# Performance work log

Hardware: AMD Instinct MI355X
Metric: run time of the kernel (lower is better)

The kernel has to match this reference:

```python
import math
import jax, jax.numpy as jnp
import numpy as np

HIDDEN = 128
NUM_REL = 48
NUM_BASES = 8
NUM_ENT = 50000
NUM_SPECIAL = 64
NUM_EDGES = 600000


def setup_inputs() -> dict:
    key = jax.random.key(0)
    ks = jax.random.split(key, 8)
    edge_index = jax.random.randint(ks[0], (2, NUM_EDGES), 0, NUM_ENT, dtype=jnp.int64)
    edge_type = jax.random.randint(ks[1], (NUM_EDGES,), 0, NUM_REL, dtype=jnp.int64)
    # node embeddings: uniform(-stdv, stdv), stdv = sqrt(6/(N+d)) as in the torch init
    stdv = math.sqrt(6.0 / (NUM_ENT + HIDDEN))
    node_embeds = jax.random.uniform(ks[2], (NUM_ENT, HIDDEN), jnp.float32, -stdv, stdv)
    # RGCN basis-decomposition params (PyG RGCNConv): weight [B, d, d], comp [R, B]
    basis = jax.random.normal(ks[3], (NUM_BASES, HIDDEN, HIDDEN), jnp.float32) * (1.0 / math.sqrt(HIDDEN))
    comp = jax.random.normal(ks[4], (NUM_REL, NUM_BASES), jnp.float32) * (1.0 / math.sqrt(NUM_BASES))
    root = jax.random.normal(ks[5], (HIDDEN, HIDDEN), jnp.float32) * (1.0 / math.sqrt(HIDDEN))
    bias = jnp.zeros((HIDDEN,), jnp.float32)
    special_emb = jax.random.normal(ks[6], (NUM_SPECIAL, HIDDEN), jnp.float32) * 0.02
    special_emb = special_emb.at[0].set(0.0)  # padding_idx=0
    return {"edge_index": edge_index, "edge_type": edge_type,
            "node_embeds": node_embeds, "basis": basis, "comp": comp,
            "root": root, "bias": bias, "special_emb": special_emb}


def rgcn_conv(x, edge_index, edge_type, basis, comp, root, bias):
    # PyG RGCNConv with basis decomposition, aggr='mean', root weight + bias.
    # W_r = sum_b comp[r, b] * basis[b]; out[n] = x[n] @ root + bias
    #        + sum_r mean_{e: type(e)=r, dst(e)=n} (x[src(e)] @ W_r)
    N = x.shape[0]
    R, B = comp.shape
    src, dst = edge_index[0], edge_index[1]
    # per-(relation, dst) in-degree for the per-relation mean aggregation
    seg = edge_type * N + dst  # [E]
    cnt = jax.ops.segment_sum(jnp.ones(src.shape[0], x.dtype), seg, num_segments=R * N)
    norm = 1.0 / jnp.maximum(cnt[seg], 1.0)  # [E]
    w = comp[edge_type] * norm[:, None]  # [E, B] per-edge basis coefficients / count
    x_src = x[src]  # [E, d] gather (dominant memory traffic)
    out = x @ root + bias  # [N, d]
    # linearity: mean over edges of (x_src @ W) == (weighted-sum of x_src) @ basis_b per basis
    for b in range(B):
        agg = jax.ops.segment_sum(x_src * w[:, b:b + 1], dst, num_segments=N)  # [N, d]
        out = out + agg @ basis[b]
    return out


def reference(edge_index, edge_type, node_embeds, basis, comp, root, bias, special_emb):
    node_out = rgcn_conv(node_embeds, edge_index, edge_type, basis, comp, root, bias)
    return jnp.concatenate([node_out, special_emb], axis=0)  # [N + S, d]
```

## Files before the change

### kernel.cpp

```cpp
#include <hip/hip_runtime.h>

#define NDIM 128
#define NBASES 8
#define KDIM 1152
#define GTILE 16
#define APITCH 1160

typedef __attribute__((ext_vector_type(8))) __bf16 bfrag;
typedef __attribute__((ext_vector_type(4))) float f32x4;

__device__ __forceinline__ float bf2f(unsigned short b) {
    return __uint_as_float(((unsigned)b) << 16);
}
__device__ __forceinline__ unsigned short f2bf(float f) {
    unsigned u = __float_as_uint(f);
    unsigned r = u + 0x7FFFu + ((u >> 16) & 1u);
    return (unsigned short)(r >> 16);
}
__device__ __forceinline__ unsigned pack2bf(float lo, float hi) {
    return (unsigned)f2bf(lo) | ((unsigned)f2bf(hi) << 16);
}
__device__ __forceinline__ float loadF(const void* p, int idx, int isf32) {
    return isf32 ? ((const float*)p)[idx] : bf2f(((const unsigned short*)p)[idx]);
}

__global__ void detect_k(const unsigned short* __restrict__ xs,
                         const int* __restrict__ ei, int* __restrict__ meta) {
    if (threadIdx.x != 0 || blockIdx.x != 0) return;
    const uint4* xv = (const uint4*)xs;
    unsigned f32m = 0;
    uint4 bx[16];
    #pragma unroll
    for (int i = 0; i < 16; ++i) bx[i] = xv[i];
    #pragma unroll
    for (int i = 0; i < 16; ++i) {
        unsigned a = bx[i].x, b = bx[i].y, c = bx[i].z, d = bx[i].w;
        f32m |= (((a & 0xFFFFu) >> 7) & 0xFFu) > 124u;
        f32m |= (((b & 0xFFFFu) >> 7) & 0xFFu) > 124u;
        f32m |= (((c & 0xFFFFu) >> 7) & 0xFFu) > 124u;
        f32m |= (((d & 0xFFFFu) >> 7) & 0xFFu) > 124u;
    }
    const uint4* ev = (const uint4*)ei;
    unsigned nzm = 0;
    for (int r = 0; r < 4; ++r) {
        uint4 be[16];
        #pragma unroll
        for (int i = 0; i < 16; ++i) be[i] = ev[r * 16 + i];
        #pragma unroll
        for (int i = 0; i < 16; ++i) nzm |= be[i].y | be[i].w;
    }
    meta[0] = f32m ? 1 : 0;
    meta[1] = nzm ? 0 : 1;
}

__global__ void misc_k(const void* __restrict__ basis, const void* __restrict__ root,
                       const void* __restrict__ se, const int* __restrict__ meta,
                       unsigned short* __restrict__ BT, void* __restrict__ out,
                       int scount, int sbase,
                       const int* __restrict__ ei, int E, int N, int* __restrict__ hist) {
    int t = blockIdx.x * 256 + threadIdx.x;
    int isf32 = meta[0];
    if (t < NDIM * KDIM) {
        int j = t / KDIM, k = t % KDIM;
        float v = (k < NBASES * NDIM) ? loadF(basis, k * NDIM + j, isf32)
                                      : loadF(root, (k - NBASES * NDIM) * NDIM + j, isf32);
        BT[t] = f2bf(v);
    } else {
        int u = t - NDIM * KDIM;
        if (u < scount) {
            float v = loadF(se, u, isf32);
            if (isf32) ((float*)out)[sbase + u] = v;
            else       ((unsigned short*)out)[sbase + u] = f2bf(v);
        } else {
            int e = u - scount;
            if (e < E) {
                int dst = meta[1] ? ei[2 * (E + e)] : ei[E + e];
                dst = min(max(dst, 0), N - 1);
                atomicAdd(&hist[dst], 1);
            }
        }
    }
}

__global__ void scanA_k(const int* __restrict__ hist, int N,
                        int* __restrict__ offsets, int* __restrict__ bsum) {
    __shared__ int s[1024];
    int tid = threadIdx.x;
    int idx = blockIdx.x * 1024 + tid;
    int v = (idx < N) ? hist[idx] : 0;
    s[tid] = v;
    __syncthreads();
    for (int off = 1; off < 1024; off <<= 1) {
        int t = 0;
        if (tid >= off) t = s[tid - off];
        __syncthreads();
        if (tid >= off) s[tid] += t;
        __syncthreads();
    }
    if (idx < N) offsets[idx] = s[tid] - v;
    if (tid == 1023) bsum[blockIdx.x] = s[1023];
}
__global__ void scanB_k(const int* __restrict__ bsum, int NB, int N,
                        int* __restrict__ bpre, int* __restrict__ offsets) {
    __shared__ int s[64];
    int tid = threadIdx.x;
    int v = (tid < NB) ? bsum[tid] : 0;
    s[tid] = v;
    __syncthreads();
    for (int off = 1; off < 64; off <<= 1) {
        int t = 0;
        if (tid >= off) t = s[tid - off];
        __syncthreads();
        if (tid >= off) s[tid] += t;
        __syncthreads();
    }
    if (tid < NB) bpre[tid] = s[tid] - v;
    if (tid == NB - 1) offsets[N] = s[tid];
}

__global__ void scatter_k(const int* __restrict__ ei, const int* __restrict__ et,
                          int E, int N, const int* __restrict__ meta,
                          const int* __restrict__ offsets, const int* __restrict__ bpre,
                          int* __restrict__ cursor, int* __restrict__ sorted) {
    int e = blockIdx.x * 256 + threadIdx.x;
    if (e >= E) return;
    int i64 = meta[1];
    int src = i64 ? ei[2 * e] : ei[e];
    int dst = i64 ? ei[2 * (E + e)] : ei[E + e];
    int rel = i64 ? et[2 * e] : et[e];
    src = min(max(src, 0), N - 1);
    dst = min(max(dst, 0), N - 1);
    rel = rel & 63;
    int pos = offsets[dst] + bpre[dst >> 10] + atomicAdd(&cursor[dst], 1);
    sorted[pos] = src | (rel << 16);
}

__global__ __launch_bounds__(1024, 8) void rgcn_main_k(
    const void* __restrict__ x, const void* __restrict__ comp,
    const void* __restrict__ bias, const unsigned short* __restrict__ BT,
    const int* __restrict__ meta, const int* __restrict__ offsets,
    const int* __restrict__ bpre,
    const int* __restrict__ sorted, void* __restrict__ out, int N)
{
    __shared__ alignas(16) unsigned short A_lds[GTILE * APITCH];
    __shared__ alignas(16) float comp_lds[48 * NBASES];
    __shared__ int cnt_lds[GTILE * 48];
    const int tid  = threadIdx.x;
    const int lane = tid & 63;
    const int wave = tid >> 6;
    const int isf32 = meta[0];

    for (int t = tid; t < 48 * NBASES; t += 1024)
        comp_lds[t] = loadF(comp, t, isf32);
    __syncthreads();

    const int nodeBase = blockIdx.x * GTILE;
    const int dl = lane & 31;
    const int eg = lane >> 5;

    {
        const int n = nodeBase + wave;
        float acc[4][4];
        #pragma unroll
        for (int b = 0; b < 4; ++b)
            #pragma unroll
            for (int i = 0; i < 4; ++i) acc[b][i] = 0.f;

        int* cnt_row = &cnt_lds[wave * 48];

        if (n < N) {
            const int start = offsets[n] + bpre[n >> 10];
            const int idx1  = n + 1;
            const int end   = offsets[idx1] + ((idx1 < N) ? bpre[idx1 >> 10] : 0);

            if (lane < 48) cnt_row[lane] = 0;
            for (int c = start + lane; c < end; c += 64)
                atomicAdd(&cnt_row[(sorted[c] >> 16) & 63], 1);
            if (lane < 48) {
                float nv = __builtin_amdgcn_rcpf(fmaxf((float)cnt_row[lane], 1.0f));
                cnt_row[lane] = __float_as_int(nv);
            }

            if (!isf32) {
                const unsigned short* xh = (const unsigned short*)x;
                if (start < end) {
                    int i0 = start + eg;
                    unsigned q0 = (i0 < end) ? (unsigned)sorted[i0] : 0u;
                    int i1 = start + 2 + eg;
                    unsigned q1 = (i1 < end) ? (unsigned)sorted[i1] : 0u;
                    uint2 xa0 = *(const uint2*)(xh + (size_t)(q0 & 0xFFFFu) * NDIM + dl * 4);
                    uint2 xa1 = *(const uint2*)(xh + (size_t)(q1 & 0xFFFFu) * NDIM + dl * 4);
                    int i2 = start + 4 + eg;
                    unsigned q2 = (i2 < end) ? (unsigned)sorted[i2] : 0u;
                    for (int c = start; c < end; c += 2) {
                        uint2 xa2 = *(const uint2*)(xh + (size_t)(q2 & 0xFFFFu) * NDIM + dl * 4);
                        int i3 = c + 6 + eg;
                        unsigned q3 = (i3 < end) ? (unsigned)sorted[i3] : 0u;

                        bool act_o = (c + eg) < end;
                        bool act_p = (c + (1 ^ eg)) < end;
                        unsigned qp = (unsigned)__shfl_xor((int)q0, 32);
                        int rel_o = (int)((q0 >> 16) & 63u);
                        int rel_p = (int)((qp >> 16) & 63u);
                        float nrm_o = act_o ? __int_as_float(cnt_row[rel_o]) : 0.f;
                        float nrm_p = act_p ? __int_as_float(cnt_row[rel_p]) : 0.f;
                        f32x4 cw_o = *(const f32x4*)&comp_lds[rel_o * NBASES + 4 * eg];
                        f32x4 cw_p = *(const f32x4*)&comp_lds[rel_p * NBASES + 4 * eg];
                        unsigned px = (unsigned)__shfl_xor((int)xa0.x, 32);
                        unsigned py = (unsigned)__shfl_xor((int)xa0.y, 32);
                        float xo[4], xq[4];
                        xo[0] = __uint_as_float(xa0.x << 16)          * nrm_o;
                        xo[1] = __uint_as_float(xa0.x & 0xFFFF0000u)  * nrm_o;
                        xo[2] = __uint_as_float(xa0.y << 16)          * nrm_o;
                        xo[3] = __uint_as_float(xa0.y & 0xFFFF0000u)  * nrm_o;
                        xq[0] = __uint_as_float(px << 16)             * nrm_p;
                        xq[1] = __uint_as_float(px & 0xFFFF0000u)     * nrm_p;
                        xq[2] = __uint_as_float(py << 16)             * nrm_p;
                        xq[3] = __uint_as_float(py & 0xFFFF0000u)     * nrm_p;
                        #pragma unroll
                        for (int b = 0; b < 4; ++b)
                            #pragma unroll
                            for (int i = 0; i < 4; ++i)
                                acc[b][i] += cw_o[b] * xo[i] + cw_p[b] * xq[i];
                        q0 = q1; q1 = q2; q2 = q3;
                        xa0 = xa1; xa1 = xa2;
                    }
                }
            } else {
                const float* xfp = (const float*)x;
                for (int c = start; c < end; c += 2) {
                    bool act_o = (c + eg) < end;
                    bool act_p = (c + (1 ^ eg)) < end;
                    int io = c + eg;
                    unsigned q0 = (io < end) ? (unsigned)sorted[io] : 0u;
                    unsigned qp = (unsigned)__shfl_xor((int)q0, 32);
                    int rel_o = (int)((q0 >> 16) & 63u);
                    int rel_p = (int)((qp >> 16) & 63u);
                    float nrm_o = act_o ? __int_as_float(cnt_row[rel_o]) : 0.f;
                    float nrm_p = act_p ? __int_as_float(cnt_row[rel_p]) : 0.f;
                    f32x4 cw_o = *(const f32x4*)&comp_lds[rel_o * NBASES + 4 * eg];
                    f32x4 cw_p = *(const f32x4*)&comp_lds[rel_p * NBASES + 4 * eg];
                    f32x4 xv = *(const f32x4*)(xfp + (size_t)(q0 & 0xFFFFu) * NDIM + dl * 4);
                    float xo[4], xq[4];
                    #pragma unroll
                    for (int i = 0; i < 4; ++i) {
                        xo[i] = xv[i] * nrm_o;
                        xq[i] = __shfl_xor(xv[i], 32) * nrm_p;
                    }
                    #pragma unroll
                    for (int b = 0; b < 4; ++b)
                        #pragma unroll
                        for (int i = 0; i < 4; ++i)
                            acc[b][i] += cw_o[b] * xo[i] + cw_p[b] * xq[i];
                }
            }
        }

        unsigned short* row = &A_lds[wave * APITCH];
        #pragma unroll
        for (int b = 0; b < 4; ++b) {
            uint2 p;
            p.x = pack2bf(acc[b][0], acc[b][1]);
            p.y = pack2bf(acc[b][2], acc[b][3]);
            *(uint2*)(row + (4 * eg + b) * NDIM + dl * 4) = p;
        }
        if (eg == 0) {
            uint2 xr = {0, 0};
            if (n < N) {
                if (!isf32) {
                    xr = *(const uint2*)((const unsigned short*)x + (size_t)n * NDIM + dl * 4);
                } else {
                    const float* xf = (const float*)x + (size_t)n * NDIM + dl * 4;
                    xr.x = pack2bf(xf[0], xf[1]);
                    xr.y = pack2bf(xf[2], xf[3]);
                }
            }
            *(uint2*)(row + NBASES * NDIM + dl * 4) = xr;
        }
    }
    __syncthreads();

    if (wave < 4) {
        const int m = lane & 15;
        const int q = lane >> 4;
        f32x4 C0 = {0,0,0,0}, C1 = {0,0,0,0};
        const unsigned short* arow = &A_lds[m * APITCH];
        const int jb = wave * 32;
        for (int ks = 0; ks < KDIM / 32; ++ks) {
            int k = ks * 32 + q * 8;
            bfrag a  = *(const bfrag*)(arow + k);
            bfrag b0 = *(const bfrag*)(BT + (size_t)(jb +  0 + m) * KDIM + k);
            bfrag b1 = *(const bfrag*)(BT + (size_t)(jb + 16 + m) * KDIM + k);
            C0 = __builtin_amdgcn_mfma_f32_16x16x32_bf16(a, b0, C0, 0, 0, 0);
            C1 = __builtin_amdgcn_mfma_f32_16x16x32_bf16(a, b1, C1, 0, 0, 0);
        }
        #pragma unroll
        for (int t = 0; t < 2; ++t) {
            f32x4 Ct = t ? C1 : C0;
            int j = jb + t * 16 + m;
            float bj = loadF(bias, j, isf32);
            #pragma unroll
            for (int r = 0; r < 4; ++r) {
                int n = nodeBase + q * 4 + r;
                if (n < N) {
                    float v = Ct[r] + bj;
                    if (isf32) ((float*)out)[(size_t)n * NDIM + j] = v;
                    else       ((unsigned short*)out)[(size_t)n * NDIM + j] = f2bf(v);
                }
            }
        }
    }
}

extern "C" void kernel_launch(void* const* d_in, const int* in_sizes, int n_in,
                              void* d_out, int out_size, void* d_ws, size_t ws_size,
                              hipStream_t stream) {
    const int* ei = (const int*)d_in[0];
    const int* et = (const int*)d_in[1];

    const int E = in_sizes[1];
    const int N = in_sizes[2] / NDIM;
    const int S = in_sizes[7] / NDIM;
    const int NB = (N + 1023) / 1024;

    char* ws = (char*)d_ws;
    size_t off = 0;
    int* meta    = (int*)(ws + off); off += 16;
    int* hist    = (int*)(ws + off); off += (size_t)N * 4;
    int* cursor  = (int*)(ws + off); off += (size_t)N * 4;
    int* offsets = (int*)(ws + off); off = (off + (size_t)(N + 1) * 4 + 15) & ~(size_t)15;
    int* bsum    = (int*)(ws + off); off += 64 * 4;
    int* bpre    = (int*)(ws + off); off += 64 * 4;
    unsigned short* BT = (unsigned short*)(ws + off); off += (size_t)NDIM * KDIM * 2;
    int* sorted  = (int*)(ws + off); off += (size_t)E * 4;

    hipMemsetAsync(hist, 0, (size_t)2 * N * 4, stream);

    detect_k<<<1, 64, 0, stream>>>((const unsigned short*)d_in[2], ei, meta);
    {
        int T = NDIM * KDIM + S * NDIM + E;
        misc_k<<<(T + 255) / 256, 256, 0, stream>>>(
            d_in[3], d_in[5], d_in[7], meta, BT, d_out, S * NDIM, N * NDIM,
            ei, E, N, hist);
    }
    scanA_k<<<NB, 1024, 0, stream>>>(hist, N, offsets, bsum);
    scanB_k<<<1, 64, 0, stream>>>(bsum, NB, N, bpre, offsets);
    scatter_k<<<(E + 255) / 256, 256, 0, stream>>>(ei, et, E, N, meta, offsets, bpre, cursor, sorted);
    rgcn_main_k<<<(N + GTILE - 1) / GTILE, 1024, 0, stream>>>(d_in[2], d_in[4], d_in[6], BT,
                                                              meta, offsets, bpre, sorted, d_out, N);
}
```

Measured before the change: 324.7 us.

## Stage neighbor gathers into LDS via async global_load_lds with double buffering

Replaces the register-prefetched bf16 neighbor gather with asynchronous global-to-LDS loads. Each wave stages eight neighbor rows at a time into double buffers, reusing the A tile rows as the second buffer, and waits on vmcnt so more loads stay in flight. The node tile is halved to 8 with 512-thread blocks, and the MFMA stage now has all 8 waves each computing 16 output columns with half the 16-row tile padded. This trades extra LDS traffic and some wasted MFMA rows for deeper memory-level parallelism and smaller blocks.

Result: slower. 530.6 us (+63.4%).

```diff
diff --git a/kernel.cpp b/kernel.cpp
--- a/kernel.cpp
+++ b/kernel.cpp
@@ -3,7 +3,7 @@
 #define NDIM 128
 #define NBASES 8
 #define KDIM 1152
-#define GTILE 16
+#define GTILE 8
 #define APITCH 1160
 
 typedef __attribute__((ext_vector_type(8))) __bf16 bfrag;
@@ -135,7 +135,7 @@
     sorted[pos] = src | (rel << 16);
 }
 
-__global__ __launch_bounds__(1024, 8) void rgcn_main_k(
+__global__ __launch_bounds__(512, 8) void rgcn_main_k(
     const void* __restrict__ x, const void* __restrict__ comp,
     const void* __restrict__ bias, const unsigned short* __restrict__ BT,
     const int* __restrict__ meta, const int* __restrict__ offsets,
@@ -143,6 +143,7 @@
     const int* __restrict__ sorted, void* __restrict__ out, int N)
 {
     __shared__ alignas(16) unsigned short A_lds[GTILE * APITCH];
+    __shared__ alignas(16) unsigned char stage_lds[GTILE * 2048];
     __shared__ alignas(16) float comp_lds[48 * NBASES];
     __shared__ int cnt_lds[GTILE * 48];
     const int tid  = threadIdx.x;
@@ -150,7 +151,7 @@
     const int wave = tid >> 6;
     const int isf32 = meta[0];
 
-    for (int t = tid; t < 48 * NBASES; t += 1024)
+    for (int t = tid; t < 48 * NBASES; t += 512)
         comp_lds[t] = loadF(comp, t, isf32);
     __syncthreads();
 
@@ -181,52 +182,70 @@
                 cnt_row[lane] = __float_as_int(nv);
             }
 
-            if (!isf32) {
+            if (!isf32 && start < end) {
                 const unsigned short* xh = (const unsigned short*)x;
-                if (start < end) {
-                    int i0 = start + eg;
-                    unsigned q0 = (i0 < end) ? (unsigned)sorted[i0] : 0u;
-                    int i1 = start + 2 + eg;
-                    unsigned q1 = (i1 < end) ? (unsigned)sorted[i1] : 0u;
-                    uint2 xa0 = *(const uint2*)(xh + (size_t)(q0 & 0xFFFFu) * NDIM + dl * 4);
-                    uint2 xa1 = *(const uint2*)(xh + (size_t)(q1 & 0xFFFFu) * NDIM + dl * 4);
-                    int i2 = start + 4 + eg;
-                    unsigned q2 = (i2 < end) ? (unsigned)sorted[i2] : 0u;
-                    for (int c = start; c < end; c += 2) {
-                        uint2 xa2 = *(const uint2*)(xh + (size_t)(q2 & 0xFFFFu) * NDIM + dl * 4);
-                        int i3 = c + 6 + eg;
-                        unsigned q3 = (i3 < end) ? (unsigned)sorted[i3] : 0u;
-
-                        bool act_o = (c + eg) < end;
-                        bool act_p = (c + (1 ^ eg)) < end;
-                        unsigned qp = (unsigned)__shfl_xor((int)q0, 32);
-                        int rel_o = (int)((q0 >> 16) & 63u);
-                        int rel_p = (int)((qp >> 16) & 63u);
-                        float nrm_o = act_o ? __int_as_float(cnt_row[rel_o]) : 0.f;
-                        float nrm_p = act_p ? __int_as_float(cnt_row[rel_p]) : 0.f;
-                        f32x4 cw_o = *(const f32x4*)&comp_lds[rel_o * NBASES + 4 * eg];
-                        f32x4 cw_p = *(const f32x4*)&comp_lds[rel_p * NBASES + 4 * eg];
-                        unsigned px = (unsigned)__shfl_xor((int)xa0.x, 32);
-                        unsigned py = (unsigned)__shfl_xor((int)xa0.y, 32);
-                        float xo[4], xq[4];
-                        xo[0] = __uint_as_float(xa0.x << 16)          * nrm_o;
-                        xo[1] = __uint_as_float(xa0.x & 0xFFFF0000u)  * nrm_o;
-                        xo[2] = __uint_as_float(xa0.y << 16)          * nrm_o;
-                        xo[3] = __uint_as_float(xa0.y & 0xFFFF0000u)  * nrm_o;
-                        xq[0] = __uint_as_float(px << 16)             * nrm_p;
-                        xq[1] = __uint_as_float(px & 0xFFFF0000u)     * nrm_p;
-                        xq[2] = __uint_as_float(py << 16)             * nrm_p;
-                        xq[3] = __uint_as_float(py & 0xFFFF0000u)     * nrm_p;
+                unsigned char* buf0 = &stage_lds[wave * 2048];
+                unsigned char* buf1 = (unsigned char*)&A_lds[wave * APITCH];
+
+                for (int w0 = start; w0 < end; w0 += 64) {
+                    int sv = (w0 + lane < end) ? sorted[w0 + lane] : 0;
+                    const int wdeg = min(64, end - w0);
+                    const int nch = (wdeg + 7) >> 3;
+
+                    #pragma unroll
+                    for (int u = 0; u < 8; ++u) {
+                        unsigned qs = (unsigned)__shfl(sv, u);
+                        unsigned src = (u < wdeg) ? (qs & 0xFFFFu) : 0u;
+                        const unsigned short* gp = xh + (size_t)src * NDIM + lane * 2;
+                        __builtin_amdgcn_global_load_lds(
+                            (const __attribute__((address_space(1))) unsigned*)gp,
+                            (__attribute__((address_space(3))) unsigned*)(buf0 + u * 256),
+                            4, 0, 0);
+                    }
+                    for (int i = 0; i < nch; ++i) {
+                        unsigned char* cur = (i & 1) ? buf1 : buf0;
+                        if (i + 1 < nch) {
+                            unsigned char* nxt = (i & 1) ? buf0 : buf1;
+                            const int cb = (i + 1) * 8;
+                            #pragma unroll
+                            for (int u = 0; u < 8; ++u) {
+                                int j = cb + u;
+                                unsigned qs = (unsigned)__shfl(sv, j & 63);
+                                unsigned src = (j < wdeg) ? (qs & 0xFFFFu) : 0u;
+                                const unsigned short* gp = xh + (size_t)src * NDIM + lane * 2;
+                                __builtin_amdgcn_global_load_lds(
+                                    (const __attribute__((address_space(1))) unsigned*)gp,
+                                    (__attribute__((address_space(3))) unsigned*)(nxt + u * 256),
+                                    4, 0, 0);
+                            }
+                            asm volatile("s_waitcnt vmcnt(8)" ::: "memory");
+                        } else {
+                            asm volatile("s_waitcnt vmcnt(0)" ::: "memory");
+                        }
+                        const int cb0 = i * 8;
                         #pragma unroll
-                        for (int b = 0; b < 4; ++b)
+                        for (int u = 0; u < 8; ++u) {
+                            int j = cb0 + u;
+                            bool act = j < wdeg;
+                            unsigned qq = (unsigned)__shfl(sv, j & 63);
+                            int rel = (int)((qq >> 16) & 63u);
+                            float norm = act ? __int_as_float(cnt_row[rel]) : 0.f;
+                            f32x4 cw = *(const f32x4*)&comp_lds[rel * NBASES + 4 * eg];
+                            uint2 xd = *(const uint2*)(cur + u * 256 + dl * 8);
+                            float xs[4];
+                            xs[0] = __uint_as_float(xd.x << 16)         * norm;
+                            xs[1] = __uint_as_float(xd.x & 0xFFFF0000u) * norm;
+                            xs[2] = __uint_as_float(xd.y << 16)         * norm;
+                            xs[3] = __uint_as_float(xd.y & 0xFFFF0000u) * norm;
                             #pragma unroll
-                            for (int i = 0; i < 4; ++i)
-                                acc[b][i] += cw_o[b] * xo[i] + cw_p[b] * xq[i];
-                        q0 = q1; q1 = q2; q2 = q3;
-                        xa0 = xa1; xa1 = xa2;
+                            for (int b = 0; b < 4; ++b)
+                                #pragma unroll
+                                for (int i2 = 0; i2 < 4; ++i2)
+                                    acc[b][i2] += cw[b] * xs[i2];
+                        }
                     }
                 }
-            } else {
+            } else if (isf32) {
                 const float* xfp = (const float*)x;
                 for (int c = start; c < end; c += 2) {
                     bool act_o = (c + eg) < end;
@@ -280,30 +299,27 @@
     }
     __syncthreads();
 
-    if (wave < 4) {
+    {
         const int m = lane & 15;
         const int q = lane >> 4;
-        f32x4 C0 = {0,0,0,0}, C1 = {0,0,0,0};
-        const unsigned short* arow = &A_lds[m * APITCH];
-        const int jb = wave * 32;
+        f32x4 C0 = {0, 0, 0, 0};
+        const unsigned short* arow = &A_lds[(m & 7) * APITCH];
+        const int jb = wave * 16;
         for (int ks = 0; ks < KDIM / 32; ++ks) {
             int k = ks * 32 + q * 8;
-            bfrag a  = *(const bfrag*)(arow + k);
-            bfrag b0 = *(const bfrag*)(BT + (size_t)(jb +  0 + m) * KDIM + k);
-            bfrag b1 = *(const bfrag*)(BT + (size_t)(jb + 16 + m) * KDIM + k);
-            C0 = __builtin_amdgcn_mfma_f32_16x16x32_bf16(a, b0, C0, 0, 0, 0);
-            C1 = __builtin_amdgcn_mfma_f32_16x16x32_bf16(a, b1, C1, 0, 0, 0);
-        }
-        #pragma unroll
-        for (int t = 0; t < 2; ++t) {
-            f32x4 Ct = t ? C1 : C0;
-            int j = jb + t * 16 + m;
-            float bj = loadF(bias, j, isf32);
-            #pragma unroll
-            for (int r = 0; r < 4; ++r) {
-                int n = nodeBase + q * 4 + r;
+            bfrag a = *(const bfrag*)(arow + k);
+            bfrag b = *(const bfrag*)(BT + (size_t)(jb + m) * KDIM + k);
+            C0 = __builtin_amdgcn_mfma_f32_16x16x32_bf16(a, b, C0, 0, 0, 0);
+        }
+        int j = jb + m;
+        float bj = loadF(bias, j, isf32);
+        #pragma unroll
+        for (int r = 0; r < 4; ++r) {
+            int row16 = q * 4 + r;
+            if (row16 < GTILE) {
+                int n = nodeBase + row16;
                 if (n < N) {
-                    float v = Ct[r] + bj;
+                    float v = C0[r] + bj;
                     if (isf32) ((float*)out)[(size_t)n * NDIM + j] = v;
                     else       ((unsigned short*)out)[(size_t)n * NDIM + j] = f2bf(v);
                 }
@@ -346,6 +362,6 @@
     scanA_k<<<NB, 1024, 0, stream>>>(hist, N, offsets, bsum);
     scanB_k<<<1, 64, 0, stream>>>(bsum, NB, N, bpre, offsets);
     scatter_k<<<(E + 255) / 256, 256, 0, stream>>>(ei, et, E, N, meta, offsets, bpre, cursor, sorted);
-    rgcn_main_k<<<(N + GTILE - 1) / GTILE, 1024, 0, stream>>>(d_in[2], d_in[4], d_in[6], BT,
-                                                              meta, offsets, bpre, sorted, d_out, N);
-}
+    rgcn_main_k<<<(N + GTILE - 1) / GTILE, 512, 0, stream>>>(d_in[2], d_in[4], d_in[6], BT,
+                                                             meta, offsets, bpre, sorted, d_out, N);
+}
```
